# Performance work log

Hardware: AMD Instinct MI355X
Metric: run time of the kernel (lower is better)

The kernel has to match this reference:

```python
import jax, jax.numpy as jnp
import numpy as np
import math

B, S, D, H = 2, 2048, 1024, 16
HD = D // H  # head_dim = 64

def setup_inputs() -> dict:
    key = jax.random.key(0)
    ks = jax.random.split(key, 11)
    def n(k, shape, scale=1.0):
        return jax.random.normal(k, shape, dtype=jnp.float32) * scale
    w_scale = 1.0 / math.sqrt(D)
    return {
        "q": n(ks[0], (B, S, D)),
        "k": n(ks[1], (B, S, D)),
        "v": n(ks[2], (B, S, D)),
        "WQ_w": n(ks[3], (D, D), w_scale),
        "WQ_b": n(ks[4], (D,), 0.01),
        "WK_w": n(ks[5], (D, D), w_scale),
        "WK_b": n(ks[6], (D,), 0.01),
        "WV_w": n(ks[7], (D, D), w_scale),
        "WV_b": n(ks[8], (D,), 0.01),
        "Wout_w": n(ks[9], (D, D), w_scale),
        "Wout_b": n(ks[10], (D,), 0.01),
    }

def reference(q, k, v, WQ_w, WQ_b, WK_w, WK_b, WV_w, WV_b, Wout_w, Wout_b):
    b, s, _ = k.shape
    # QKV projections (torch Linear: x @ W.T + b; here weights stored [in, out])
    qh = (q @ WQ_w + WQ_b).reshape(b, -1, H, HD).transpose(0, 2, 1, 3)  # [b,h,s,hd]
    kh = (k @ WK_w + WK_b).reshape(b, -1, H, HD).transpose(0, 2, 1, 3)
    vh = (v @ WV_w + WV_b).reshape(b, -1, H, HD).transpose(0, 2, 1, 3)
    # naive attention: full [b,h,s,s] score matrix
    scores = jnp.einsum("bhqd,bhkd->bhqk", qh, kh) / math.sqrt(HD)
    attn = jax.nn.softmax(scores, axis=-1)
    out = jnp.einsum("bhqk,bhkd->bhqd", attn, vh)
    concat = out.transpose(0, 2, 1, 3).reshape(b, -1, H * HD)  # [b,s,inner_dim]
    return concat @ Wout_w + Wout_b
```

## Files before the change

### kernel.cpp

```cpp
#include <hip/hip_runtime.h>
#include <hip/hip_bf16.h>
#include <stdint.h>

typedef __attribute__((ext_vector_type(8))) short bf16x8;
typedef __attribute__((ext_vector_type(4))) short short4v;
typedef __attribute__((ext_vector_type(4))) float f32x4;

#define MFMA16x16x32 __builtin_amdgcn_mfma_f32_16x16x32_bf16

__device__ __forceinline__ short f2b(float f) {
  union { float f; uint32_t u; } x;
  x.f = f;
  uint32_t u = x.u;
  uint32_t r = (u + 0x7FFFu + ((u >> 16) & 1u)) >> 16;
  return (short)(uint16_t)r;
}

__device__ __forceinline__ uint32_t cvt_pk_bf16(float lo, float hi) {
  uint32_t r;
  asm volatile("v_cvt_pk_bf16_f32 %0, %1, %2" : "=v"(r) : "v"(lo), "v"(hi));
  return r;
}
__device__ __forceinline__ float exp2_fast(float x) {
  float r;
  asm volatile("v_exp_f32 %0, %1" : "=v"(r) : "v"(x));
  return r;
}
__device__ __forceinline__ bf16x8 cvt8(const float4 a, const float4 b) {
  union { uint32_t u[4]; bf16x8 v; } o;
  o.u[0] = cvt_pk_bf16(a.x, a.y);
  o.u[1] = cvt_pk_bf16(a.z, a.w);
  o.u[2] = cvt_pk_bf16(b.x, b.y);
  o.u[3] = cvt_pk_bf16(b.z, b.w);
  return o.v;
}

__device__ __forceinline__ void async_copy16(const void* g, void* l) {
  __builtin_amdgcn_global_load_lds(
      (const __attribute__((address_space(1))) void*)g,
      (__attribute__((address_space(3))) void*)l, 16, 0, 0);
}

__global__ void cvt3_kernel(const float* __restrict__ x0,
                            const float* __restrict__ x1,
                            const float* __restrict__ x2,
                            short* __restrict__ y0,
                            short* __restrict__ y1,
                            short* __restrict__ y2) {
  const int t = blockIdx.y;
  const float* x = (t == 0) ? x0 : (t == 1) ? x1 : x2;
  short* yp = (t == 0) ? y0 : (t == 1) ? y1 : y2;
  const int i = blockIdx.x * blockDim.x + threadIdx.x;
  const float4 a = ((const float4*)x)[2 * i];
  const float4 b = ((const float4*)x)[2 * i + 1];
  ((bf16x8*)yp)[i] = cvt8(a, b);
}

__global__ void transpose4_kernel(const float* __restrict__ W0,
                                  const float* __restrict__ W1,
                                  const float* __restrict__ W2,
                                  const float* __restrict__ W3,
                                  short* __restrict__ Wt) {
  __shared__ short tile[64][72];
  const int mat = blockIdx.z;
  const float* W = (mat == 0) ? W0 : (mat == 1) ? W1 : (mat == 2) ? W2 : W3;
  short* Wo = Wt + (size_t)mat * 1024 * 1024;
  const int r0 = blockIdx.y * 64;
  const int c0 = blockIdx.x * 64;
  const int t = threadIdx.x;
#pragma unroll
  for (int i = 0; i < 4; ++i) {
    const int lin = i * 1024 + t * 4;
    const int r = lin >> 6, c = lin & 63;
    const float4 v = *(const float4*)&W[(size_t)(r0 + r) * 1024 + c0 + c];
    tile[r][c + 0] = f2b(v.x);
    tile[r][c + 1] = f2b(v.y);
    tile[r][c + 2] = f2b(v.z);
    tile[r][c + 3] = f2b(v.w);
  }
  __syncthreads();
#pragma unroll
  for (int i = 0; i < 2; ++i) {
    const int lin = i * 2048 + t * 8;
    const int r = lin >> 6, c = lin & 63;
    bf16x8 ov;
#pragma unroll
    for (int jj = 0; jj < 8; ++jj) ov[jj] = tile[c + jj][r];
    *(bf16x8*)&Wo[(size_t)(c0 + r) * 1024 + r0 + c] = ov;
  }
}

__launch_bounds__(256, 2)
__global__ void gemm_qkv_kernel(const short* __restrict__ A0,
                                const short* __restrict__ A1,
                                const short* __restrict__ A2,
                                const short* __restrict__ WtBase,
                                const float* __restrict__ b0,
                                const float* __restrict__ b1,
                                const float* __restrict__ b2,
                                short* __restrict__ C0,
                                short* __restrict__ C1,
                                short* __restrict__ Vt,
                                int ybase) {
  const int K = 1024;
  __shared__ short As[128 * 64];
  __shared__ short Bs[128 * 64];

  const int y = blockIdx.y + ybase;
  const short* A = (y == 0) ? A0 : (y == 1) ? A1 : A2;
  const short* Wt = WtBase + (size_t)y * 1024 * 1024;
  const float* bias = (y == 0) ? b0 : (y == 1) ? b1 : b2;

  const int tm = blockIdx.x & 31;
  const int tn = blockIdx.x >> 5;
  const int m0 = tm * 128, n0 = tn * 128;

  const int tid = threadIdx.x;
  const int lane = tid & 63;
  const int w = tid >> 6;
  const int wr = w >> 1, wc = w & 1;
  const int hi = lane >> 4, cc = lane & 15;
  const int srow = lane >> 3, schunk = lane & 7;

  f32x4 acc[4][4] = {};

  for (int kt = 0; kt < 16; ++kt) {
    const int k0 = kt * 64;
#pragma unroll
    for (int i = 0; i < 4; ++i) {
      const int ri = w * 4 + i;
      const int row = ri * 8 + srow;
      const int gch = schunk ^ (row & 7);
      async_copy16(A + (size_t)(m0 + row) * K + (k0 + gch * 8), &As[ri * 512]);
      async_copy16(Wt + (size_t)(n0 + row) * K + (k0 + gch * 8), &Bs[ri * 512]);
    }
    __syncthreads();
#pragma unroll
    for (int kk = 0; kk < 2; ++kk) {
      bf16x8 af[4], bfr[4];
#pragma unroll
      for (int x = 0; x < 4; ++x) {
        const int gch = kk * 4 + hi;
        const int rowA = wr * 64 + x * 16 + cc;
        af[x] = *(const bf16x8*)&As[rowA * 64 + ((gch ^ (rowA & 7)) << 3)];
        const int rowB = wc * 64 + x * 16 + cc;
        bfr[x] = *(const bf16x8*)&Bs[rowB * 64 + ((gch ^ (rowB & 7)) << 3)];
      }
#pragma unroll
      for (int x = 0; x < 4; ++x)
#pragma unroll
        for (int yy = 0; yy < 4; ++yy)
          acc[x][yy] = MFMA16x16x32(af[x], bfr[yy], acc[x][yy], 0, 0, 0);
    }
    __syncthreads();
  }

  short* Cout = (y == 0) ? C0 : C1;
#pragma unroll
  for (int x = 0; x < 4; ++x) {
    const int rbase = m0 + wr * 64 + x * 16 + (hi << 2);
#pragma unroll
    for (int yy = 0; yy < 4; ++yy) {
      const int col = n0 + wc * 64 + yy * 16 + cc;
      const float bv = bias[col];
      if (y == 2) {
        const int b = rbase >> 11, s = rbase & 2047;
        const int hh = col >> 6, d = col & 63;
        short4v pack;
#pragma unroll
        for (int r = 0; r < 4; ++r) pack[r] = f2b(acc[x][yy][r] + bv);
        *(short4v*)&Vt[((size_t)(b * 16 + hh) * 64 + d) * 2048 + s] = pack;
      } else {
#pragma unroll
        for (int r = 0; r < 4; ++r)
          Cout[(size_t)(rbase + r) * 1024 + col] = f2b(acc[x][yy][r] + bv);
      }
    }
  }
}

__launch_bounds__(256, 2)
__global__ void gemm_out_kernel(const short* __restrict__ A,
                                const short* __restrict__ Wt,
                                const float* __restrict__ bias,
                                float* __restrict__ C) {
  const int N = 1024, K = 1024;
  __shared__ short As[128 * 64];
  __shared__ short Bs[128 * 64];

  const int tm = blockIdx.x & 31;
  const int tn = blockIdx.x >> 5;
  const int m0 = tm * 128, n0 = tn * 128;

  const int tid = threadIdx.x;
  const int lane = tid & 63;
  const int w = tid >> 6;
  const int wr = w >> 1, wc = w & 1;
  const int hi = lane >> 4, cc = lane & 15;
  const int srow = lane >> 3, schunk = lane & 7;

  f32x4 acc[4][4] = {};

  for (int kt = 0; kt < 16; ++kt) {
    const int k0 = kt * 64;
#pragma unroll
    for (int i = 0; i < 4; ++i) {
      const int ri = w * 4 + i;
      const int row = ri * 8 + srow;
      const int gch = schunk ^ (row & 7);
      async_copy16(A + (size_t)(m0 + row) * K + (k0 + gch * 8), &As[ri * 512]);
      async_copy16(Wt + (size_t)(n0 + row) * K + (k0 + gch * 8), &Bs[ri * 512]);
    }
    __syncthreads();
#pragma unroll
    for (int kk = 0; kk < 2; ++kk) {
      bf16x8 af[4], bfr[4];
#pragma unroll
      for (int x = 0; x < 4; ++x) {
        const int gch = kk * 4 + hi;
        const int rowA = wr * 64 + x * 16 + cc;
        af[x] = *(const bf16x8*)&As[rowA * 64 + ((gch ^ (rowA & 7)) << 3)];
        const int rowB = wc * 64 + x * 16 + cc;
        bfr[x] = *(const bf16x8*)&Bs[rowB * 64 + ((gch ^ (rowB & 7)) << 3)];
      }
#pragma unroll
      for (int x = 0; x < 4; ++x)
#pragma unroll
        for (int yy = 0; yy < 4; ++yy)
          acc[x][yy] = MFMA16x16x32(af[x], bfr[yy], acc[x][yy], 0, 0, 0);
    }
    __syncthreads();
  }

#pragma unroll
  for (int x = 0; x < 4; ++x) {
    const int rbase = m0 + wr * 64 + x * 16 + (hi << 2);
#pragma unroll
    for (int yy = 0; yy < 4; ++yy) {
      const int col = n0 + wc * 64 + yy * 16 + cc;
      const float bv = bias[col];
#pragma unroll
      for (int r = 0; r < 4; ++r)
        C[(size_t)(rbase + r) * N + col] = acc[x][yy][r] + bv;
    }
  }
}

__launch_bounds__(256, 2)
__global__ void attn_kernel(const short* __restrict__ qh,
                            const short* __restrict__ kh,
                            const short* __restrict__ Vt,
                            short* __restrict__ concat) {
  const int S = 2048;
  const float CL2 = 0.18033688011112042f;
  __shared__ short Ks[2][64 * 64];
  __shared__ short Vs[2][64 * 64];
  __shared__ short Ps[4 * 32 * 64];

  const int qb = blockIdx.x;
  const int h = blockIdx.y;
  const int b = blockIdx.z;
  const int tid = threadIdx.x, lane = tid & 63, w = tid >> 6;
  const int hi = lane >> 4, cc = lane & 15;

  const size_t rowbase = (size_t)b * S;
  const int q0 = qb * 128 + w * 32;

  bf16x8 qf[2][2];
#pragma unroll
  for (int aq = 0; aq < 2; ++aq)
#pragma unroll
    for (int kk = 0; kk < 2; ++kk) {
      const int col = h * 64 + kk * 32 + hi * 8;
      qf[aq][kk] =
          *(const bf16x8*)&qh[(rowbase + q0 + aq * 16 + cc) * 1024 + col];
    }

  f32x4 oacc[2][4] = {};
  float l[2] = {0.f, 0.f};

  const short* Vth = Vt + (size_t)(b * 16 + h) * 64 * 2048;
  short* Pw = &Ps[w * 2048];
  const int srow = lane >> 3, schunk = lane & 7;
  const int e0 = (cc >> 3) & 1;

#pragma unroll
  for (int i = 0; i < 2; ++i) {
    const int ri = w * 2 + i;
    const int row = ri * 8 + srow;
    const int gch = schunk ^ (row & 7);
    async_copy16(&kh[(rowbase + row) * 1024 + h * 64 + gch * 8], &Ks[0][ri * 512]);
    async_copy16(&Vth[(size_t)row * 2048 + gch * 8], &Vs[0][ri * 512]);
  }
  __syncthreads();

  for (int t = 0; t < S / 64; ++t) {
    const int cur = t & 1;
    if (t + 1 < S / 64) {
      const int kv0 = (t + 1) * 64;
#pragma unroll
      for (int i = 0; i < 2; ++i) {
        const int ri = w * 2 + i;
        const int row = ri * 8 + srow;
        const int gch = schunk ^ (row & 7);
        async_copy16(&kh[(rowbase + kv0 + row) * 1024 + h * 64 + gch * 8],
                     &Ks[cur ^ 1][ri * 512]);
        async_copy16(&Vth[(size_t)row * 2048 + kv0 + gch * 8],
                     &Vs[cur ^ 1][ri * 512]);
      }
    }

    f32x4 sacc[2][4] = {};
#pragma unroll
    for (int kk = 0; kk < 2; ++kk) {
      bf16x8 kf[4];
#pragma unroll
      for (int n = 0; n < 4; ++n) {
        const int row = n * 16 + cc;
        const int ch = (kk * 4 + hi) ^ (cc & 7);
        kf[n] = *(const bf16x8*)&Ks[cur][row * 64 + (ch << 3)];
      }
#pragma unroll
      for (int aq = 0; aq < 2; ++aq)
#pragma unroll
        for (int n = 0; n < 4; ++n)
          sacc[aq][n] = MFMA16x16x32(kf[n], qf[aq][kk], sacc[aq][n], 0, 0, 0);
    }

#pragma unroll
    for (int aq = 0; aq < 2; ++aq) {
      const int qrow = aq * 16 + cc;
#pragma unroll
      for (int n = 0; n < 4; ++n) {
        const float p0 = exp2_fast(sacc[aq][n][0] * CL2);
        const float p1 = exp2_fast(sacc[aq][n][1] * CL2);
        const float p2 = exp2_fast(sacc[aq][n][2] * CL2);
        const float p3 = exp2_fast(sacc[aq][n][3] * CL2);
        l[aq] += (p0 + p1) + (p2 + p3);
        const uint32_t u0 = cvt_pk_bf16(p0, p1);
        const uint32_t u1 = cvt_pk_bf16(p2, p3);
        const int chunk = (2 * n + (hi >> 1)) ^ (cc & 7);
        const int base = qrow * 64 + (chunk << 3) + ((hi & 1) << 2);
        *(uint32_t*)&Pw[base + (e0 << 1)] = e0 ? u1 : u0;
        *(uint32_t*)&Pw[base + ((e0 ^ 1) << 1)] = e0 ? u0 : u1;
      }
    }

#pragma unroll
    for (int kvh = 0; kvh < 2; ++kvh) {
      const int ch = (kvh * 4 + hi) ^ (cc & 7);
      bf16x8 pf[2], vf[4];
#pragma unroll
      for (int aq = 0; aq < 2; ++aq)
        pf[aq] = *(const bf16x8*)&Pw[(aq * 16 + cc) * 64 + (ch << 3)];
#pragma unroll
      for (int n = 0; n < 4; ++n) {
        const int row = n * 16 + cc;
        vf[n] = *(const bf16x8*)&Vs[cur][row * 64 + (ch << 3)];
      }
#pragma unroll
      for (int aq = 0; aq < 2; ++aq)
#pragma unroll
        for (int n = 0; n < 4; ++n)
          oacc[aq][n] = MFMA16x16x32(vf[n], pf[aq], oacc[aq][n], 0, 0, 0);
    }
    __syncthreads();
  }

#pragma unroll
  for (int aq = 0; aq < 2; ++aq) {
    float lv = l[aq];
    lv += __shfl_xor(lv, 16);
    lv += __shfl_xor(lv, 32);
    const float inv = 1.0f / lv;
    const size_t grow = rowbase + q0 + aq * 16 + cc;
#pragma unroll
    for (int n = 0; n < 4; ++n)
#pragma unroll
      for (int r = 0; r < 4; ++r) {
        const int d = n * 16 + hi * 4 + r;
        concat[grow * 1024 + h * 64 + d] = f2b(oacc[aq][n][r] * inv);
      }
  }
}

extern "C" void kernel_launch(void* const* d_in, const int* in_sizes, int n_in,
                              void* d_out, int out_size, void* d_ws, size_t ws_size,
                              hipStream_t stream) {
  const float* q = (const float*)d_in[0];
  const float* k = (const float*)d_in[1];
  const float* v = (const float*)d_in[2];
  const float* WQ = (const float*)d_in[3];
  const float* bQ = (const float*)d_in[4];
  const float* WK = (const float*)d_in[5];
  const float* bK = (const float*)d_in[6];
  const float* WV = (const float*)d_in[7];
  const float* bV = (const float*)d_in[8];
  const float* WO = (const float*)d_in[9];
  const float* bO = (const float*)d_in[10];

  char* ws = (char*)d_ws;
  const size_t MB = 1024 * 1024;
  short* Wt = (short*)ws;
  short* xq = (short*)(ws + 8 * MB);
  short* xk = (short*)(ws + 16 * MB);
  short* xv = (short*)(ws + 24 * MB);
  short* qh = (short*)(ws + 32 * MB);
  short* kh = (short*)(ws + 40 * MB);
  short* Vt = xq;
  short* concat = xk;

  transpose4_kernel<<<dim3(16, 16, 4), 256, 0, stream>>>(WQ, WK, WV, WO, Wt);
  cvt3_kernel<<<dim3(2048, 3), 256, 0, stream>>>(q, k, v, xq, xk, xv);
  gemm_qkv_kernel<<<dim3(256, 2), 256, 0, stream>>>(
      xq, xk, xv, Wt, bQ, bK, bV, qh, kh, Vt, 0);
  gemm_qkv_kernel<<<dim3(256, 1), 256, 0, stream>>>(
      xq, xk, xv, Wt, bQ, bK, bV, qh, kh, Vt, 2);
  attn_kernel<<<dim3(16, 16, 2), 256, 0, stream>>>(qh, kh, Vt, concat);
  gemm_out_kernel<<<256, 256, 0, stream>>>(concat, Wt + 3 * MB, bO,
                                           (float*)d_out);
}
```

Before: 137.2 us.

## Merge prep kernels and halve attention block size to two waves

The weight-transpose and activation-convert kernels are merged into one launch, with the conversion blocks each handling eight chunks. The attention kernel now uses 128 threads covering 64 query rows per block, twice as many blocks, and a smaller P buffer. It also raises wave priority around the MFMA groups. The aim is to save a launch, give the GPU more attention blocks to schedule, and favour matrix issue. The cost is that each K/V tile is reused by fewer query rows, so K/V traffic per query doubles.

```diff
diff --git a/kernel.cpp b/kernel.cpp
--- a/kernel.cpp
+++ b/kernel.cpp
@@ -41,52 +41,56 @@
       (__attribute__((address_space(3))) void*)l, 16, 0, 0);
 }
 
-__global__ void cvt3_kernel(const float* __restrict__ x0,
-                            const float* __restrict__ x1,
-                            const float* __restrict__ x2,
-                            short* __restrict__ y0,
-                            short* __restrict__ y1,
-                            short* __restrict__ y2) {
-  const int t = blockIdx.y;
-  const float* x = (t == 0) ? x0 : (t == 1) ? x1 : x2;
-  short* yp = (t == 0) ? y0 : (t == 1) ? y1 : y2;
-  const int i = blockIdx.x * blockDim.x + threadIdx.x;
-  const float4 a = ((const float4*)x)[2 * i];
-  const float4 b = ((const float4*)x)[2 * i + 1];
-  ((bf16x8*)yp)[i] = cvt8(a, b);
-}
-
-__global__ void transpose4_kernel(const float* __restrict__ W0,
-                                  const float* __restrict__ W1,
-                                  const float* __restrict__ W2,
-                                  const float* __restrict__ W3,
-                                  short* __restrict__ Wt) {
+__global__ void prep_kernel(const float* __restrict__ W0,
+                            const float* __restrict__ W1,
+                            const float* __restrict__ W2,
+                            const float* __restrict__ W3,
+                            const float* __restrict__ q,
+                            const float* __restrict__ k,
+                            const float* __restrict__ v,
+                            short* __restrict__ Wt,
+                            short* __restrict__ xq,
+                            short* __restrict__ xk,
+                            short* __restrict__ xv) {
   __shared__ short tile[64][72];
-  const int mat = blockIdx.z;
-  const float* W = (mat == 0) ? W0 : (mat == 1) ? W1 : (mat == 2) ? W2 : W3;
-  short* Wo = Wt + (size_t)mat * 1024 * 1024;
-  const int r0 = blockIdx.y * 64;
-  const int c0 = blockIdx.x * 64;
+  const int z = blockIdx.z;
   const int t = threadIdx.x;
-#pragma unroll
-  for (int i = 0; i < 4; ++i) {
-    const int lin = i * 1024 + t * 4;
-    const int r = lin >> 6, c = lin & 63;
-    const float4 v = *(const float4*)&W[(size_t)(r0 + r) * 1024 + c0 + c];
-    tile[r][c + 0] = f2b(v.x);
-    tile[r][c + 1] = f2b(v.y);
-    tile[r][c + 2] = f2b(v.z);
-    tile[r][c + 3] = f2b(v.w);
-  }
-  __syncthreads();
-#pragma unroll
-  for (int i = 0; i < 2; ++i) {
-    const int lin = i * 2048 + t * 8;
-    const int r = lin >> 6, c = lin & 63;
-    bf16x8 ov;
-#pragma unroll
-    for (int jj = 0; jj < 8; ++jj) ov[jj] = tile[c + jj][r];
-    *(bf16x8*)&Wo[(size_t)(c0 + r) * 1024 + r0 + c] = ov;
+  if (z < 4) {
+    const float* W = (z == 0) ? W0 : (z == 1) ? W1 : (z == 2) ? W2 : W3;
+    short* Wo = Wt + (size_t)z * 1024 * 1024;
+    const int r0 = blockIdx.y * 64;
+    const int c0 = blockIdx.x * 64;
+#pragma unroll
+    for (int i = 0; i < 4; ++i) {
+      const int lin = i * 1024 + t * 4;
+      const int r = lin >> 6, c = lin & 63;
+      const float4 vv = *(const float4*)&W[(size_t)(r0 + r) * 1024 + c0 + c];
+      tile[r][c + 0] = f2b(vv.x);
+      tile[r][c + 1] = f2b(vv.y);
+      tile[r][c + 2] = f2b(vv.z);
+      tile[r][c + 3] = f2b(vv.w);
+    }
+    __syncthreads();
+#pragma unroll
+    for (int i = 0; i < 2; ++i) {
+      const int lin = i * 2048 + t * 8;
+      const int r = lin >> 6, c = lin & 63;
+      bf16x8 ov;
+#pragma unroll
+      for (int jj = 0; jj < 8; ++jj) ov[jj] = tile[c + jj][r];
+      *(bf16x8*)&Wo[(size_t)(c0 + r) * 1024 + r0 + c] = ov;
+    }
+  } else {
+    const float* x = (z == 4) ? q : (z == 5) ? k : v;
+    short* yp = (z == 4) ? xq : (z == 5) ? xk : xv;
+    const int base = (blockIdx.y * 16 + blockIdx.x) * 256 + t;
+#pragma unroll
+    for (int j = 0; j < 8; ++j) {
+      const int i = base + j * 65536;
+      const float4 a = ((const float4*)x)[2 * i];
+      const float4 b = ((const float4*)x)[2 * i + 1];
+      ((bf16x8*)yp)[i] = cvt8(a, b);
+    }
   }
 }
 
@@ -246,7 +250,7 @@
   }
 }
 
-__launch_bounds__(256, 2)
+__launch_bounds__(128, 2)
 __global__ void attn_kernel(const short* __restrict__ qh,
                             const short* __restrict__ kh,
                             const short* __restrict__ Vt,
@@ -255,7 +259,7 @@
   const float CL2 = 0.18033688011112042f;
   __shared__ short Ks[2][64 * 64];
   __shared__ short Vs[2][64 * 64];
-  __shared__ short Ps[4 * 32 * 64];
+  __shared__ short Ps[2][32 * 64];
 
   const int qb = blockIdx.x;
   const int h = blockIdx.y;
@@ -264,7 +268,7 @@
   const int hi = lane >> 4, cc = lane & 15;
 
   const size_t rowbase = (size_t)b * S;
-  const int q0 = qb * 128 + w * 32;
+  const int q0 = qb * 64 + w * 32;
 
   bf16x8 qf[2][2];
 #pragma unroll
@@ -280,13 +284,13 @@
   float l[2] = {0.f, 0.f};
 
   const short* Vth = Vt + (size_t)(b * 16 + h) * 64 * 2048;
-  short* Pw = &Ps[w * 2048];
+  short* Pw = &Ps[w][0];
   const int srow = lane >> 3, schunk = lane & 7;
   const int e0 = (cc >> 3) & 1;
 
 #pragma unroll
-  for (int i = 0; i < 2; ++i) {
-    const int ri = w * 2 + i;
+  for (int i = 0; i < 4; ++i) {
+    const int ri = w * 4 + i;
     const int row = ri * 8 + srow;
     const int gch = schunk ^ (row & 7);
     async_copy16(&kh[(rowbase + row) * 1024 + h * 64 + gch * 8], &Ks[0][ri * 512]);
@@ -299,8 +303,8 @@
     if (t + 1 < S / 64) {
       const int kv0 = (t + 1) * 64;
 #pragma unroll
-      for (int i = 0; i < 2; ++i) {
-        const int ri = w * 2 + i;
+      for (int i = 0; i < 4; ++i) {
+        const int ri = w * 4 + i;
         const int row = ri * 8 + srow;
         const int gch = schunk ^ (row & 7);
         async_copy16(&kh[(rowbase + kv0 + row) * 1024 + h * 64 + gch * 8],
@@ -320,11 +324,13 @@
         const int ch = (kk * 4 + hi) ^ (cc & 7);
         kf[n] = *(const bf16x8*)&Ks[cur][row * 64 + (ch << 3)];
       }
+      __builtin_amdgcn_s_setprio(1);
 #pragma unroll
       for (int aq = 0; aq < 2; ++aq)
 #pragma unroll
         for (int n = 0; n < 4; ++n)
           sacc[aq][n] = MFMA16x16x32(kf[n], qf[aq][kk], sacc[aq][n], 0, 0, 0);
+      __builtin_amdgcn_s_setprio(0);
     }
 
 #pragma unroll
@@ -358,11 +364,13 @@
         const int row = n * 16 + cc;
         vf[n] = *(const bf16x8*)&Vs[cur][row * 64 + (ch << 3)];
       }
+      __builtin_amdgcn_s_setprio(1);
 #pragma unroll
       for (int aq = 0; aq < 2; ++aq)
 #pragma unroll
         for (int n = 0; n < 4; ++n)
           oacc[aq][n] = MFMA16x16x32(vf[n], pf[aq], oacc[aq][n], 0, 0, 0);
+      __builtin_amdgcn_s_setprio(0);
     }
     __syncthreads();
   }
@@ -410,13 +418,13 @@
   short* Vt = xq;
   short* concat = xk;
 
-  transpose4_kernel<<<dim3(16, 16, 4), 256, 0, stream>>>(WQ, WK, WV, WO, Wt);
-  cvt3_kernel<<<dim3(2048, 3), 256, 0, stream>>>(q, k, v, xq, xk, xv);
+  prep_kernel<<<dim3(16, 16, 7), 256, 0, stream>>>(WQ, WK, WV, WO, q, k, v,
+                                                   Wt, xq, xk, xv);
   gemm_qkv_kernel<<<dim3(256, 2), 256, 0, stream>>>(
       xq, xk, xv, Wt, bQ, bK, bV, qh, kh, Vt, 0);
   gemm_qkv_kernel<<<dim3(256, 1), 256, 0, stream>>>(
       xq, xk, xv, Wt, bQ, bK, bV, qh, kh, Vt, 2);
-  attn_kernel<<<dim3(16, 16, 2), 256, 0, stream>>>(qh, kh, Vt, concat);
+  attn_kernel<<<dim3(32, 16, 2), 128, 0, stream>>>(qh, kh, Vt, concat);
   gemm_out_kernel<<<256, 256, 0, stream>>>(concat, Wt + 3 * MB, bO,
                                            (float*)d_out);
 }
```

After: 138.5 us. Within noise of the previous version (+1.0%).
